# Kernel optimization log

Hardware: AMD Instinct MI355X
Metric: run time of the kernel (lower is better)

## Reference

```python
import jax, jax.numpy as jnp
import numpy as np

L, D, H, V, B, S = 12, 768, 12, 50257, 1, 2048
F = 4 * D
HD = D // H
EPS = 1e-5
NEG = -1e38


def setup_inputs() -> dict:
    key = jax.random.key(0)
    ks = jax.random.split(key, 12)
    s = 0.02
    f32 = jnp.float32
    return {
        "x": jax.random.normal(ks[0], (B, S, D), f32),
        "ln1_g": jnp.ones((L, D), f32), "ln1_b": jnp.zeros((L, D), f32),
        "Wq": jax.random.normal(ks[1], (L, D, D), f32) * s,
        "Wk": jax.random.normal(ks[2], (L, D, D), f32) * s,
        "Wv": jax.random.normal(ks[3], (L, D, D), f32) * s,
        "Wo": jax.random.normal(ks[4], (L, D, D), f32) * s,
        "bo": jnp.zeros((L, D), f32),
        "ln2_g": jnp.ones((L, D), f32), "ln2_b": jnp.zeros((L, D), f32),
        "Wfc": jax.random.normal(ks[5], (L, D, F), f32) * s,
        "bfc": jnp.zeros((L, F), f32),
        "Wp": jax.random.normal(ks[6], (L, F, D), f32) * s,
        "bp": jnp.zeros((L, D), f32),
        "lnf_g": jnp.ones((D,), f32), "lnf_b": jnp.zeros((D,), f32),
        "Wlm": jax.random.normal(ks[7], (D, V), f32) * s,
    }


def _ln(h, g, b):
    mu = h.mean(-1, keepdims=True)
    var = ((h - mu) ** 2).mean(-1, keepdims=True)
    return (h - mu) * jax.lax.rsqrt(var + EPS) * g + b


def reference(x, ln1_g, ln1_b, Wq, Wk, Wv, Wo, bo, ln2_g, ln2_b,
              Wfc, bfc, Wp, bp, lnf_g, lnf_b, Wlm):
    Bx, Sx, Dx = x.shape
    # additive causal mask, NOTE: original has no 1/sqrt(head_dim) scaling
    mask = (1.0 - jnp.tril(jnp.ones((Sx, Sx), x.dtype))) * NEG

    def block(h, p):
        g1, b1, wq, wk, wv, wo, bo_, g2, b2, wfc, bfc_, wp, bp_ = p
        hn = _ln(h, g1, b1)
        def heads(w):  # [B,S,D] -> [B,H,S,hd]
            return (hn @ w).reshape(Bx, Sx, H, HD).transpose(0, 2, 1, 3)
        q, k, v = heads(wq), heads(wk), heads(wv)
        scores = jnp.einsum('bhqd,bhkd->bhqk', q, k) + mask
        probs = jax.nn.softmax(scores, axis=-1)
        attn = jnp.einsum('bhqk,bhkd->bhqd', probs, v)
        attn = attn.transpose(0, 2, 1, 3).reshape(Bx, Sx, Dx)
        h = h + attn @ wo + bo_
        hn2 = _ln(h, g2, b2)
        ff = jax.nn.gelu(hn2 @ wfc + bfc_, approximate=False) @ wp + bp_
        return h + ff, None

    h, _ = jax.lax.scan(
        block, x,
        (ln1_g, ln1_b, Wq, Wk, Wv, Wo, bo, ln2_g, ln2_b, Wfc, bfc, Wp, bp))
    return _ln(h, lnf_g, lnf_b) @ Wlm
```

## Files before the change

kernel.cpp:

```cpp
#include <hip/hip_runtime.h>
#include <hip/hip_bf16.h>
#include <math.h>

typedef unsigned short ushort;
typedef __attribute__((ext_vector_type(8))) short short8;
typedef __attribute__((ext_vector_type(4))) short short4v;
typedef __attribute__((ext_vector_type(4))) float f4v;

constexpr int SEQ = 2048;
constexpr int DM  = 768;
constexpr int NH  = 12;
constexpr int HDM = 64;
constexpr int FF  = 3072;
constexpr int NL  = 12;
constexpr int NV  = 50257;
constexpr int NVP = 50432;

__device__ inline ushort f2bf(float f) {
    union { float f; unsigned u; } v; v.f = f;
    unsigned r = v.u + 0x7fffu + ((v.u >> 16) & 1u);
    return (ushort)(r >> 16);
}

__device__ __forceinline__ void gld16(const ushort* g, ushort* l) {
    __builtin_amdgcn_global_load_lds(
        (const __attribute__((address_space(1))) void*)g,
        (__attribute__((address_space(3))) void*)l, 16, 0, 0);
}

__global__ __launch_bounds__(256) void ln_kernel(const float* __restrict__ x,
                                                 const float* __restrict__ g,
                                                 const float* __restrict__ b,
                                                 ushort* __restrict__ out) {
    int row = blockIdx.x;
    int t = threadIdx.x;
    const float* xr = x + (size_t)row * DM;
    float v0 = xr[t], v1 = xr[t + 256], v2 = xr[t + 512];
    float s = v0 + v1 + v2;
    float s2 = v0 * v0 + v1 * v1 + v2 * v2;
    for (int m = 1; m < 64; m <<= 1) { s += __shfl_xor(s, m); s2 += __shfl_xor(s2, m); }
    __shared__ float ls[4], ls2[4];
    int w = t >> 6;
    if ((t & 63) == 0) { ls[w] = s; ls2[w] = s2; }
    __syncthreads();
    s = ls[0] + ls[1] + ls[2] + ls[3];
    s2 = ls2[0] + ls2[1] + ls2[2] + ls2[3];
    float mu = s * (1.0f / DM);
    float var = s2 * (1.0f / DM) - mu * mu;
    float rs = rsqrtf(var + 1e-5f);
    ushort* o = out + (size_t)row * DM;
    o[t]       = f2bf((v0 - mu) * rs * g[t]       + b[t]);
    o[t + 256] = f2bf((v1 - mu) * rs * g[t + 256] + b[t + 256]);
    o[t + 512] = f2bf((v2 - mu) * rs * g[t + 512] + b[t + 512]);
}

struct CvtArgs {
    const float* src[7];
    ushort*      dst[7];
    long inL[7], outL[7];
    int  K[7], N[7], tk[7], tn[7];
    int  base[8];
};

__global__ __launch_bounds__(256) void cvt_all(CvtArgs a) {
    __shared__ ushort T[64][72];
    int idx = blockIdx.x;
    int seg = 0;
    #pragma unroll
    for (int i = 1; i < 7; ++i) if (idx >= a.base[i]) seg = i;
    int local = idx - a.base[seg];
    int K = a.K[seg], N = a.N[seg];
    int tk = a.tk[seg], tn = a.tn[seg];
    int k_t = local % tk;
    int rst = local / tk;
    int n_t = rst % tn;
    int l   = rst / tn;
    const float* ip = a.src[seg] + (size_t)l * a.inL[seg];
    ushort* op      = a.dst[seg] + (size_t)l * a.outL[seg];
    int kb = k_t * 64, nb = n_t * 64;
    int t = threadIdx.x;
    int nl = t & 63, ks = (t >> 6) * 16;
    int n = nb + nl;
    #pragma unroll
    for (int j = 0; j < 16; ++j) {
        float f = (n < N) ? ip[(size_t)(kb + ks + j) * N + n] : 0.f;
        T[nl][ks + j] = f2bf(f);
    }
    __syncthreads();
    int r = t >> 2, c4 = (t & 3) * 16;
    *(short8*)(op + (size_t)(nb + r) * K + kb + c4)     = *(const short8*)&T[r][c4];
    *(short8*)(op + (size_t)(nb + r) * K + kb + c4 + 8) = *(const short8*)&T[r][c4 + 8];
}

template <int BM, int BN, int EPI, bool DB, bool SWZ>
__global__ __launch_bounds__(256, 2) void gemmT(const ushort* __restrict__ A,
                                                const ushort* __restrict__ Bt,
                                                const float* __restrict__ bias,
                                                const float* __restrict__ res,
                                                void* __restrict__ outp,
                                                ushort* __restrict__ vt,
                                                int M, int N, int K, int ldOut) {
    constexpr int FM = BM / 32;
    constexpr int FN = BN / 32;
    constexpr int NBUF = DB ? 2 : 1;
    constexpr int ASZ = BM * 64;
    constexpr int BSZ = BN * 64;
    __shared__ ushort As[NBUF * ASZ];
    __shared__ ushort Bs[NBUF * BSZ];
    int tid = threadIdx.x, lane = tid & 63, wave = tid >> 6;
    int wm = (wave >> 1) * (BM / 2), wn = (wave & 1) * (BN / 2);
    int mBase, nBase;
    if constexpr (SWZ) {
        int gx = gridDim.x;
        int nwg = gx * gridDim.y;
        int flat = blockIdx.y * gx + blockIdx.x;
        int xcd = flat & 7, idx = flat >> 3;
        int q = nwg >> 3, r = nwg & 7;
        int wg = (xcd < r ? xcd * (q + 1) : r * (q + 1) + (xcd - r) * q) + idx;
        mBase = (wg % gx) * BM;
        nBase = (wg / gx) * BN;
    } else {
        mBase = blockIdx.x * BM;
        nBase = blockIdx.y * BN;
    }
    int lr = lane & 15, lg = lane >> 4;
    int swz = (lr & 7) << 3;

    f4v acc[FM][FN];
    #pragma unroll
    for (int i = 0; i < FM; ++i)
        #pragma unroll
        for (int j = 0; j < FN; ++j) acc[i][j] = (f4v){0.f, 0.f, 0.f, 0.f};

    int cBase = wave * 64 + lane;

    auto stage = [&](int kb, int buf) {
        #pragma unroll
        for (int i = 0; i < BM / 32; ++i) {
            int c = i * 256 + cBase;
            int row = c >> 3;
            int kc = (c & 7) ^ (row & 7);
            gld16(A + (size_t)(mBase + row) * K + kb + kc * 8,
                  As + buf * ASZ + (size_t)(i * 256 + wave * 64) * 8);
        }
        #pragma unroll
        for (int i = 0; i < BN / 32; ++i) {
            int c = i * 256 + cBase;
            int row = c >> 3;
            int kc = (c & 7) ^ (row & 7);
            gld16(Bt + (size_t)(nBase + row) * K + kb + kc * 8,
                  Bs + buf * BSZ + (size_t)(i * 256 + wave * 64) * 8);
        }
    };
    auto compute = [&](int buf) {
        #pragma unroll
        for (int kk = 0; kk < 2; ++kk) {
            short8 a[FM], b[FN];
            #pragma unroll
            for (int fr = 0; fr < FM; ++fr)
                a[fr] = *(const short8*)(As + buf * ASZ + (wm + fr * 16 + lr) * 64 + ((((kk * 4 + lg) << 3)) ^ swz));
            #pragma unroll
            for (int fc = 0; fc < FN; ++fc)
                b[fc] = *(const short8*)(Bs + buf * BSZ + (wn + fc * 16 + lr) * 64 + ((((kk * 4 + lg) << 3)) ^ swz));
            #pragma unroll
            for (int fr = 0; fr < FM; ++fr)
                #pragma unroll
                for (int fc = 0; fc < FN; ++fc)
                    acc[fr][fc] = __builtin_amdgcn_mfma_f32_16x16x32_bf16(a[fr], b[fc], acc[fr][fc], 0, 0, 0);
        }
    };

    if constexpr (DB) {
        stage(0, 0);
        __syncthreads();
        int cur = 0;
        for (int kb = 0; kb < K; kb += 64) {
            if (kb + 64 < K) stage(kb + 64, cur ^ 1);
            compute(cur);
            __syncthreads();
            cur ^= 1;
        }
    } else {
        for (int kb = 0; kb < K; kb += 64) {
            stage(kb, 0);
            __syncthreads();
            compute(0);
            __syncthreads();
        }
    }

    if constexpr (EPI == 4) {
        if (nBase < 1536) {
            #pragma unroll
            for (int fr = 0; fr < FM; ++fr)
                #pragma unroll
                for (int fc = 0; fc < FN; ++fc)
                    #pragma unroll
                    for (int r = 0; r < 4; ++r) {
                        int row = mBase + wm + fr * 16 + 4 * lg + r;
                        int col = nBase + wn + fc * 16 + lr;
                        ((ushort*)outp)[(size_t)row * ldOut + col] = f2bf(acc[fr][fc][r]);
                    }
        } else {
            #pragma unroll
            for (int fr = 0; fr < FM; ++fr)
                #pragma unroll
                for (int fc = 0; fc < FN; ++fc) {
                    short4v pk;
                    #pragma unroll
                    for (int r = 0; r < 4; ++r) pk[r] = (short)f2bf(acc[fr][fc][r]);
                    int d  = nBase - 1536 + wn + fc * 16 + lr;
                    int m0 = mBase + wm + fr * 16 + 4 * lg;
                    *(short4v*)(vt + (size_t)d * SEQ + m0) = pk;
                }
        }
        return;
    }

    #pragma unroll
    for (int fr = 0; fr < FM; ++fr)
        #pragma unroll
        for (int fc = 0; fc < FN; ++fc)
            #pragma unroll
            for (int r = 0; r < 4; ++r) {
                int row = mBase + wm + fr * 16 + 4 * lg + r;
                int col = nBase + wn + fc * 16 + lr;
                float v = acc[fr][fc][r];
                if constexpr (EPI == 0) {
                    ((ushort*)outp)[(size_t)row * ldOut + col] = f2bf(v);
                } else if constexpr (EPI == 1) {
                    v += bias[col] + res[(size_t)row * ldOut + col];
                    ((float*)outp)[(size_t)row * ldOut + col] = v;
                } else if constexpr (EPI == 2) {
                    v += bias[col];
                    v = 0.5f * v * (1.f + erff(v * 0.70710678118f));
                    ((ushort*)outp)[(size_t)row * ldOut + col] = f2bf(v);
                } else {
                    if (col < N) ((float*)outp)[(size_t)row * ldOut + col] = v;
                }
            }
}

__global__ __launch_bounds__(128) void attn_v7(const ushort* __restrict__ Qg,
                                               const ushort* __restrict__ Kg,
                                               const ushort* __restrict__ Vt,
                                               ushort* __restrict__ Og) {
    __shared__ ushort Ks[2 * 4096];
    __shared__ ushort Vs[2 * 4096];
    __shared__ ushort Ps[2 * 1024];
    int tid = threadIdx.x, lane = tid & 63, wave = tid >> 6;
    int flat = blockIdx.x;
    int qt   = (SEQ / 32) - 1 - (flat / NH);
    int head = flat % NH;
    int lr = lane & 15, lg = lane >> 4;
    int qr0 = qt * 32 + wave * 16;
    int hoff = head * HDM;
    int swz = (lr & 7) << 3;
    int ktiles = (qt * 32 + 31) / 64 + 1;

    short8 qf0 = *(const short8*)(Qg + (size_t)(qr0 + lr) * 2304 + hoff + lg * 8);
    short8 qf1 = *(const short8*)(Qg + (size_t)(qr0 + lr) * 2304 + hoff + 32 + lg * 8);

    const f4v fz = {0.f, 0.f, 0.f, 0.f};
    f4v o[4];
    o[0] = fz; o[1] = fz; o[2] = fz; o[3] = fz;
    float mrow[4] = {-1e30f, -1e30f, -1e30f, -1e30f};
    float lsum[4] = {0.f, 0.f, 0.f, 0.f};

    auto stageKV = [&](int kb, int buf) {
        #pragma unroll
        for (int j = 0; j < 4; ++j) {
            int cc = j * 128 + wave * 64 + lane;
            int row = cc >> 3;
            int kc = (cc & 7) ^ (row & 7);
            gld16(Kg + (size_t)(kb * 64 + row) * 2304 + hoff + kc * 8,
                  Ks + buf * 4096 + (size_t)(j * 128 + wave * 64) * 8);
            gld16(Vt + (size_t)(hoff + row) * SEQ + kb * 64 + kc * 8,
                  Vs + buf * 4096 + (size_t)(j * 128 + wave * 64) * 8);
        }
    };

    stageKV(0, 0);
    __syncthreads();
    int cur = 0;

    for (int kb = 0; kb < ktiles; ++kb) {
        if (kb + 1 < ktiles) stageKV(kb + 1, cur ^ 1);

        f4v s[4];
        #pragma unroll
        for (int n = 0; n < 4; ++n) {
            const ushort* kr = Ks + cur * 4096 + (n * 16 + lr) * 64;
            short8 k0 = *(const short8*)(kr + ((lg << 3) ^ swz));
            short8 k1 = *(const short8*)(kr + ((((4 + lg) << 3)) ^ swz));
            f4v z = fz;
            z = __builtin_amdgcn_mfma_f32_16x16x32_bf16(qf0, k0, z, 0, 0, 0);
            s[n] = __builtin_amdgcn_mfma_f32_16x16x32_bf16(qf1, k1, z, 0, 0, 0);
        }
        if (kb == ktiles - 1) {
            #pragma unroll
            for (int n = 0; n < 4; ++n)
                #pragma unroll
                for (int r = 0; r < 4; ++r) {
                    int col = kb * 64 + n * 16 + lr;
                    int row = qr0 + 4 * lg + r;
                    if (col > row) s[n][r] = -1e38f;
                }
        }

        int sub = lr & 7, hi = lr >> 3;
        #pragma unroll
        for (int r = 0; r < 4; ++r) {
            float mx = fmaxf(fmaxf(s[0][r], s[1][r]), fmaxf(s[2][r], s[3][r]));
            mx = fmaxf(mx, __shfl_xor(mx, 1));
            mx = fmaxf(mx, __shfl_xor(mx, 2));
            mx = fmaxf(mx, __shfl_xor(mx, 4));
            mx = fmaxf(mx, __shfl_xor(mx, 8));
            float mnew = fmaxf(mrow[r], mx);
            float corr = __expf(mrow[r] - mnew);
            float ps0 = __expf(s[0][r] - mnew);
            float ps1 = __expf(s[1][r] - mnew);
            float ps2 = __expf(s[2][r] - mnew);
            float ps3 = __expf(s[3][r] - mnew);
            float rs = ps0 + ps1 + ps2 + ps3;
            rs += __shfl_xor(rs, 1);
            rs += __shfl_xor(rs, 2);
            rs += __shfl_xor(rs, 4);
            rs += __shfl_xor(rs, 8);
            lsum[r] = lsum[r] * corr + rs;
            mrow[r] = mnew;
            o[0][r] *= corr; o[1][r] *= corr; o[2][r] *= corr; o[3][r] *= corr;
            int prow = 4 * lg + r;
            ushort* pb = Ps + wave * 1024 + prow * 64;
            int px = prow & 7;
            pb[(((0 + hi) ^ px) << 3) | sub] = f2bf(ps0);
            pb[(((2 + hi) ^ px) << 3) | sub] = f2bf(ps1);
            pb[(((4 + hi) ^ px) << 3) | sub] = f2bf(ps2);
            pb[(((6 + hi) ^ px) << 3) | sub] = f2bf(ps3);
        }
        __syncthreads();

        #pragma unroll
        for (int kk = 0; kk < 2; ++kk) {
            short8 pa = *(const short8*)(Ps + wave * 1024 + lr * 64 + ((((kk * 4 + lg) << 3)) ^ swz));
            #pragma unroll
            for (int dn = 0; dn < 4; ++dn) {
                short8 vb = *(const short8*)(Vs + cur * 4096 + (dn * 16 + lr) * 64 + ((((kk * 4 + lg) << 3)) ^ swz));
                o[dn] = __builtin_amdgcn_mfma_f32_16x16x32_bf16(pa, vb, o[dn], 0, 0, 0);
            }
        }
        __syncthreads();
        cur ^= 1;
    }

    #pragma unroll
    for (int dn = 0; dn < 4; ++dn)
        #pragma unroll
        for (int r = 0; r < 4; ++r) {
            int row = qr0 + 4 * lg + r;
            Og[(size_t)row * DM + hoff + dn * 16 + lr] = f2bf(o[dn][r] / lsum[r]);
        }
}

template <int EPI>
__global__ __launch_bounds__(256) void gemm64(const ushort* __restrict__ A,
                                              const float* __restrict__ B,
                                              const float* __restrict__ bias,
                                              const float* __restrict__ res,
                                              void* __restrict__ outp,
                                              int M, int N, int K) {
    __shared__ ushort As[64][64];
    __shared__ ushort Bs[64][72];
    int tid = threadIdx.x;
    int lane = tid & 63, wave = tid >> 6;
    int wm = (wave >> 1) * 32, wn = (wave & 1) * 32;
    int mBase = blockIdx.x * 64, nBase = blockIdx.y * 64;
    int lr = lane & 15, lg = lane >> 4;

    const f4v fz = {0.f, 0.f, 0.f, 0.f};
    f4v acc[2][2];
    acc[0][0] = fz; acc[0][1] = fz; acc[1][0] = fz; acc[1][1] = fz;

    int ar = tid >> 2, ac = (tid & 3) * 16;
    int br = tid >> 2, bc = (tid & 3) * 16;

    for (int kb = 0; kb < K; kb += 64) {
        const short8* ag = (const short8*)(A + (size_t)(mBase + ar) * K + kb + ac);
        *(short8*)&As[ar][ac]     = ag[0];
        *(short8*)&As[ar][ac + 8] = ag[1];
        if constexpr (EPI == 3) {
            #pragma unroll
            for (int j = 0; j < 16; ++j) {
                int col = nBase + bc + j;
                float f = (col < N) ? B[(size_t)(kb + br) * N + col] : 0.f;
                Bs[bc + j][br] = f2bf(f);
            }
        } else {
            const float4* bg = (const float4*)(B + (size_t)(kb + br) * N + nBase + bc);
            float fv[16];
            *(float4*)&fv[0]  = bg[0];
            *(float4*)&fv[4]  = bg[1];
            *(float4*)&fv[8]  = bg[2];
            *(float4*)&fv[12] = bg[3];
            #pragma unroll
            for (int j = 0; j < 16; ++j) Bs[bc + j][br] = f2bf(fv[j]);
        }
        __syncthreads();
        #pragma unroll
        for (int kk = 0; kk < 2; ++kk) {
            short8 a0 = *(const short8*)&As[wm + lr][kk * 32 + lg * 8];
            short8 a1 = *(const short8*)&As[wm + 16 + lr][kk * 32 + lg * 8];
            short8 b0 = *(const short8*)&Bs[wn + lr][kk * 32 + lg * 8];
            short8 b1 = *(const short8*)&Bs[wn + 16 + lr][kk * 32 + lg * 8];
            acc[0][0] = __builtin_amdgcn_mfma_f32_16x16x32_bf16(a0, b0, acc[0][0], 0, 0, 0);
            acc[0][1] = __builtin_amdgcn_mfma_f32_16x16x32_bf16(a0, b1, acc[0][1], 0, 0, 0);
            acc[1][0] = __builtin_amdgcn_mfma_f32_16x16x32_bf16(a1, b0, acc[1][0], 0, 0, 0);
            acc[1][1] = __builtin_amdgcn_mfma_f32_16x16x32_bf16(a1, b1, acc[1][1], 0, 0, 0);
        }
        __syncthreads();
    }

    #pragma unroll
    for (int fm = 0; fm < 2; ++fm)
        #pragma unroll
        for (int fn = 0; fn < 2; ++fn)
            #pragma unroll
            for (int r = 0; r < 4; ++r) {
                int row = mBase + wm + fm * 16 + 4 * lg + r;
                int col = nBase + wn + fn * 16 + lr;
                float v = acc[fm][fn][r];
                if constexpr (EPI == 0) {
                    ((ushort*)outp)[(size_t)row * N + col] = f2bf(v);
                } else if constexpr (EPI == 1) {
                    v += bias[col] + res[(size_t)row * N + col];
                    ((float*)outp)[(size_t)row * N + col] = v;
                } else if constexpr (EPI == 2) {
                    v += bias[col];
                    v = 0.5f * v * (1.f + erff(v * 0.70710678118f));
                    ((ushort*)outp)[(size_t)row * N + col] = f2bf(v);
                } else {
                    if (col < N) ((float*)outp)[(size_t)row * N + col] = v;
                }
            }
}

__global__ __launch_bounds__(256) void attn_stage(const ushort* __restrict__ Qg,
                                                  const ushort* __restrict__ Kg,
                                                  const ushort* __restrict__ Vg,
                                                  ushort* __restrict__ Og,
                                                  int ld) {
    __shared__ ushort Ks[64][64];
    __shared__ ushort Vs[64][72];
    __shared__ ushort Ps[4][16][64];
    int tid = threadIdx.x, lane = tid & 63, wave = tid >> 6;
    int qb = blockIdx.x, head = blockIdx.y;
    int lr = lane & 15, lg = lane >> 4;
    int qr0 = qb * 64 + wave * 16;
    size_t hoff = (size_t)head * HDM;

    short8 qf0 = *(const short8*)(Qg + (size_t)(qr0 + lr) * ld + hoff + lg * 8);
    short8 qf1 = *(const short8*)(Qg + (size_t)(qr0 + lr) * ld + hoff + 32 + lg * 8);

    const f4v fz = {0.f, 0.f, 0.f, 0.f};
    f4v o[4];
    o[0] = fz; o[1] = fz; o[2] = fz; o[3] = fz;
    float mrow[4] = {-1e30f, -1e30f, -1e30f, -1e30f};
    float lsum[4] = {0.f, 0.f, 0.f, 0.f};

    int r_ = tid >> 2, c_ = (tid & 3) * 16;

    for (int kb = 0; kb <= qb; ++kb) {
        const short8* kg = (const short8*)(Kg + (size_t)(kb * 64 + r_) * ld + hoff + c_);
        *(short8*)&Ks[r_][c_]     = kg[0];
        *(short8*)&Ks[r_][c_ + 8] = kg[1];
        const short8* vg = (const short8*)(Vg + (size_t)(kb * 64 + r_) * ld + hoff + c_);
        short8 v0 = vg[0], v1 = vg[1];
        #pragma unroll
        for (int j = 0; j < 8; ++j) {
            Vs[c_ + j][r_]     = (ushort)v0[j];
            Vs[c_ + 8 + j][r_] = (ushort)v1[j];
        }
        __syncthreads();

        f4v s[4];
        #pragma unroll
        for (int n = 0; n < 4; ++n) {
            short8 k0 = *(const short8*)&Ks[n * 16 + lr][lg * 8];
            short8 k1 = *(const short8*)&Ks[n * 16 + lr][32 + lg * 8];
            f4v z = fz;
            z = __builtin_amdgcn_mfma_f32_16x16x32_bf16(qf0, k0, z, 0, 0, 0);
            s[n] = __builtin_amdgcn_mfma_f32_16x16x32_bf16(qf1, k1, z, 0, 0, 0);
        }
        if (kb == qb) {
            #pragma unroll
            for (int n = 0; n < 4; ++n)
                #pragma unroll
                for (int r = 0; r < 4; ++r) {
                    int col = kb * 64 + n * 16 + lr;
                    int row = qr0 + 4 * lg + r;
                    if (col > row) s[n][r] = -1e38f;
                }
        }

        #pragma unroll
        for (int r = 0; r < 4; ++r) {
            float mx = fmaxf(fmaxf(s[0][r], s[1][r]), fmaxf(s[2][r], s[3][r]));
            mx = fmaxf(mx, __shfl_xor(mx, 1));
            mx = fmaxf(mx, __shfl_xor(mx, 2));
            mx = fmaxf(mx, __shfl_xor(mx, 4));
            mx = fmaxf(mx, __shfl_xor(mx, 8));
            float mnew = fmaxf(mrow[r], mx);
            float corr = __expf(mrow[r] - mnew);
            float ps0 = __expf(s[0][r] - mnew);
            float ps1 = __expf(s[1][r] - mnew);
            float ps2 = __expf(s[2][r] - mnew);
            float ps3 = __expf(s[3][r] - mnew);
            float rs = ps0 + ps1 + ps2 + ps3;
            rs += __shfl_xor(rs, 1);
            rs += __shfl_xor(rs, 2);
            rs += __shfl_xor(rs, 4);
            rs += __shfl_xor(rs, 8);
            lsum[r] = lsum[r] * corr + rs;
            mrow[r] = mnew;
            o[0][r] *= corr; o[1][r] *= corr; o[2][r] *= corr; o[3][r] *= corr;
            Ps[wave][4 * lg + r][0 * 16 + lr] = f2bf(ps0);
            Ps[wave][4 * lg + r][1 * 16 + lr] = f2bf(ps1);
            Ps[wave][4 * lg + r][2 * 16 + lr] = f2bf(ps2);
            Ps[wave][4 * lg + r][3 * 16 + lr] = f2bf(ps3);
        }
        __syncthreads();

        #pragma unroll
        for (int kk = 0; kk < 2; ++kk) {
            short8 pa = *(const short8*)&Ps[wave][lr][kk * 32 + lg * 8];
            #pragma unroll
            for (int dn = 0; dn < 4; ++dn) {
                short8 vb = *(const short8*)&Vs[dn * 16 + lr][kk * 32 + lg * 8];
                o[dn] = __builtin_amdgcn_mfma_f32_16x16x32_bf16(pa, vb, o[dn], 0, 0, 0);
            }
        }
        __syncthreads();
    }

    #pragma unroll
    for (int dn = 0; dn < 4; ++dn)
        #pragma unroll
        for (int r = 0; r < 4; ++r) {
            int row = qr0 + 4 * lg + r;
            Og[(size_t)row * DM + hoff + dn * 16 + lr] = f2bf(o[dn][r] / lsum[r]);
        }
}

extern "C" void kernel_launch(void* const* d_in, const int* in_sizes, int n_in,
                              void* d_out, int out_size, void* d_ws, size_t ws_size,
                              hipStream_t stream) {
    const float* x     = (const float*)d_in[0];
    const float* ln1_g = (const float*)d_in[1];
    const float* ln1_b = (const float*)d_in[2];
    const float* Wq    = (const float*)d_in[3];
    const float* Wk    = (const float*)d_in[4];
    const float* Wv    = (const float*)d_in[5];
    const float* Wo    = (const float*)d_in[6];
    const float* bo    = (const float*)d_in[7];
    const float* ln2_g = (const float*)d_in[8];
    const float* ln2_b = (const float*)d_in[9];
    const float* Wfc   = (const float*)d_in[10];
    const float* bfc   = (const float*)d_in[11];
    const float* Wp    = (const float*)d_in[12];
    const float* bp    = (const float*)d_in[13];
    const float* lnf_g = (const float*)d_in[14];
    const float* lnf_b = (const float*)d_in[15];
    const float* Wlm   = (const float*)d_in[16];

    dim3 blk(256);

    size_t offs[12];
    size_t need = 0;
    size_t sizes[11] = {
        (size_t)SEQ * DM * 4,
        (size_t)SEQ * DM * 2,
        (size_t)SEQ * 2304 * 2,
        (size_t)SEQ * DM * 2,
        (size_t)SEQ * FF * 2,
        (size_t)DM * SEQ * 2,
        (size_t)NL * 2304 * DM * 2,
        (size_t)NL * DM * DM * 2,
        (size_t)NL * FF * DM * 2,
        (size_t)NL * DM * FF * 2,
        (size_t)NVP * DM * 2,
    };
    for (int i = 0; i < 11; ++i) { offs[i] = need; need += sizes[i]; }
    offs[11] = need;

    if (ws_size >= need) {
        char* ws = (char*)d_ws;
        float*  h    = (float*)(ws + offs[0]);
        ushort* hn   = (ushort*)(ws + offs[1]);
        ushort* qkv  = (ushort*)(ws + offs[2]);
        ushort* ab_  = (ushort*)(ws + offs[3]);
        ushort* fb_  = (ushort*)(ws + offs[4]);
        ushort* vt   = (ushort*)(ws + offs[5]);
        ushort* qkvw = (ushort*)(ws + offs[6]);
        ushort* wow  = (ushort*)(ws + offs[7]);
        ushort* fcw  = (ushort*)(ws + offs[8]);
        ushort* wpw  = (ushort*)(ws + offs[9]);
        ushort* lmw  = (ushort*)(ws + offs[10]);

        hipMemcpyAsync(h, x, (size_t)SEQ * DM * 4, hipMemcpyDeviceToDevice, stream);

        CvtArgs ca;
        const float* srcs[7] = {Wq, Wk, Wv, Wo, Wfc, Wp, Wlm};
        ushort* dsts[7] = {qkvw, qkvw + DM * DM, qkvw + 2 * DM * DM, wow, fcw, wpw, lmw};
        long inLs[7]  = {(long)DM * DM, (long)DM * DM, (long)DM * DM, (long)DM * DM,
                         (long)DM * FF, (long)FF * DM, 0};
        long outLs[7] = {(long)2304 * DM, (long)2304 * DM, (long)2304 * DM, (long)DM * DM,
                         (long)FF * DM, (long)DM * FF, 0};
        int Ks_[7] = {DM, DM, DM, DM, DM, FF, DM};
        int Ns_[7] = {DM, DM, DM, DM, FF, DM, NV};
        int tks[7] = {12, 12, 12, 12, 12, 48, 12};
        int tns[7] = {12, 12, 12, 12, 48, 12, NVP / 64};
        int lays[7] = {NL, NL, NL, NL, NL, NL, 1};
        int total = 0;
        for (int i = 0; i < 7; ++i) {
            ca.src[i] = srcs[i]; ca.dst[i] = dsts[i];
            ca.inL[i] = inLs[i]; ca.outL[i] = outLs[i];
            ca.K[i] = Ks_[i]; ca.N[i] = Ns_[i]; ca.tk[i] = tks[i]; ca.tn[i] = tns[i];
            ca.base[i] = total;
            total += tks[i] * tns[i] * lays[i];
        }
        ca.base[7] = total;
        cvt_all<<<dim3(total), blk, 0, stream>>>(ca);

        for (int l = 0; l < NL; ++l) {
            const ushort* qw = qkvw + (size_t)l * 2304 * DM;
            ln_kernel<<<SEQ, blk, 0, stream>>>(h, ln1_g + l * DM, ln1_b + l * DM, hn);
            gemmT<64, 64, 4, true, false><<<dim3(32, 36), blk, 0, stream>>>(hn, qw, nullptr, nullptr, qkv, vt, SEQ, 2304, DM, 2304);
            attn_v7<<<dim3((SEQ / 32) * NH), dim3(128), 0, stream>>>(qkv, qkv + 768, vt, ab_);
            gemmT<64, 64, 1, true, false><<<dim3(32, 12), blk, 0, stream>>>(ab_, wow + (size_t)l * DM * DM, bo + l * DM, h, h, nullptr, SEQ, DM, DM, DM);
            ln_kernel<<<SEQ, blk, 0, stream>>>(h, ln2_g + l * DM, ln2_b + l * DM, hn);
            gemmT<64, 64, 2, true, false><<<dim3(32, 48), blk, 0, stream>>>(hn, fcw + (size_t)l * FF * DM, bfc + l * FF, nullptr, fb_, nullptr, SEQ, FF, DM, FF);
            gemmT<64, 64, 1, true, false><<<dim3(32, 12), blk, 0, stream>>>(fb_, wpw + (size_t)l * DM * FF, bp + l * DM, h, h, nullptr, SEQ, DM, FF, DM);
        }
        ln_kernel<<<SEQ, blk, 0, stream>>>(h, lnf_g, lnf_b, hn);
        gemmT<128, 256, 3, false, true><<<dim3(16, NVP / 256), blk, 0, stream>>>(hn, lmw, nullptr, nullptr, d_out, nullptr, SEQ, NV, DM, NV);
        return;
    }

    char* ws = (char*)d_ws;
    float*  h   = (float*)ws;   ws += (size_t)SEQ * DM * 4;
    ushort* hn  = (ushort*)ws;  ws += (size_t)SEQ * DM * 2;
    ushort* qb_ = (ushort*)ws;  ws += (size_t)SEQ * DM * 2;
    ushort* kb_ = (ushort*)ws;  ws += (size_t)SEQ * DM * 2;
    ushort* vb_ = (ushort*)ws;  ws += (size_t)SEQ * DM * 2;
    ushort* ab_ = (ushort*)ws;  ws += (size_t)SEQ * DM * 2;
    ushort* fb_ = (ushort*)ws;  ws += (size_t)SEQ * FF * 2;

    hipMemcpyAsync(h, x, (size_t)SEQ * DM * 4, hipMemcpyDeviceToDevice, stream);

    dim3 gdd(SEQ / 64, DM / 64);
    dim3 gdf(SEQ / 64, FF / 64);
    dim3 gda(SEQ / 64, NH);
    dim3 gdl(SEQ / 64, (NV + 63) / 64);

    for (int l = 0; l < NL; ++l) {
        ln_kernel<<<SEQ, blk, 0, stream>>>(h, ln1_g + l * DM, ln1_b + l * DM, hn);
        gemm64<0><<<gdd, blk, 0, stream>>>(hn, Wq + (size_t)l * DM * DM, nullptr, nullptr, qb_, SEQ, DM, DM);
        gemm64<0><<<gdd, blk, 0, stream>>>(hn, Wk + (size_t)l * DM * DM, nullptr, nullptr, kb_, SEQ, DM, DM);
        gemm64<0><<<gdd, blk, 0, stream>>>(hn, Wv + (size_t)l * DM * DM, nullptr, nullptr, vb_, SEQ, DM, DM);
        attn_stage<<<gda, blk, 0, stream>>>(qb_, kb_, vb_, ab_, DM);
        gemm64<1><<<gdd, blk, 0, stream>>>(ab_, Wo + (size_t)l * DM * DM, bo + l * DM, h, h, SEQ, DM, DM);
        ln_kernel<<<SEQ, blk, 0, stream>>>(h, ln2_g + l * DM, ln2_b + l * DM, hn);
        gemm64<2><<<gdf, blk, 0, stream>>>(hn, Wfc + (size_t)l * DM * FF, bfc + l * FF, nullptr, fb_, SEQ, FF, DM);
        gemm64<1><<<gdd, blk, 0, stream>>>(fb_, Wp + (size_t)l * FF * DM, bp + l * DM, h, h, SEQ, DM, FF);
    }
    ln_kernel<<<SEQ, blk, 0, stream>>>(h, lnf_g, lnf_b, hn);
    gemm64<3><<<gdl, blk, 0, stream>>>(hn, Wlm, nullptr, nullptr, d_out, SEQ, NV, DM);
}
```

Baseline: 2.518 ms.

## Split-K the FFN down-projection and retile the LM-head GEMM

```diff
diff --git a/kernel.cpp b/kernel.cpp
--- a/kernel.cpp
+++ b/kernel.cpp
@@ -14,7 +14,7 @@
 constexpr int FF  = 3072;
 constexpr int NL  = 12;
 constexpr int NV  = 50257;
-constexpr int NVP = 50432;
+constexpr int NVP = 50496;
 
 __device__ inline ushort f2bf(float f) {
     union { float f; unsigned u; } v; v.f = f;
@@ -54,6 +54,24 @@
     o[t + 512] = f2bf((v2 - mu) * rs * g[t + 512] + b[t + 512]);
 }
 
+__global__ __launch_bounds__(256) void spk_reduce(const float* __restrict__ p,
+                                                  const float* __restrict__ bias,
+                                                  float* __restrict__ h) {
+    int idx = blockIdx.x * 256 + threadIdx.x;
+    int col4 = idx % (DM / 4);
+    float4 a  = ((const float4*)h)[idx];
+    float4 b  = ((const float4*)bias)[col4];
+    float4 s0 = ((const float4*)p)[idx];
+    float4 s1 = ((const float4*)(p + (size_t)SEQ * DM))[idx];
+    float4 s2 = ((const float4*)(p + 2 * (size_t)SEQ * DM))[idx];
+    float4 s3 = ((const float4*)(p + 3 * (size_t)SEQ * DM))[idx];
+    a.x += b.x + s0.x + s1.x + s2.x + s3.x;
+    a.y += b.y + s0.y + s1.y + s2.y + s3.y;
+    a.z += b.z + s0.z + s1.z + s2.z + s3.z;
+    a.w += b.w + s0.w + s1.w + s2.w + s3.w;
+    ((float4*)h)[idx] = a;
+}
+
 struct CvtArgs {
     const float* src[7];
     ushort*      dst[7];
@@ -92,14 +110,15 @@
     *(short8*)(op + (size_t)(nb + r) * K + kb + c4 + 8) = *(const short8*)&T[r][c4 + 8];
 }
 
-template <int BM, int BN, int EPI, bool DB, bool SWZ>
-__global__ __launch_bounds__(256, 2) void gemmT(const ushort* __restrict__ A,
-                                                const ushort* __restrict__ Bt,
-                                                const float* __restrict__ bias,
-                                                const float* __restrict__ res,
-                                                void* __restrict__ outp,
-                                                ushort* __restrict__ vt,
-                                                int M, int N, int K, int ldOut) {
+template <int BM, int BN, int EPI, bool DB, bool SWZ, int MINW>
+__global__ __launch_bounds__(256, MINW) void gemmT(const ushort* __restrict__ A,
+                                                   const ushort* __restrict__ Bt,
+                                                   const float* __restrict__ bias,
+                                                   const float* __restrict__ res,
+                                                   void* __restrict__ outp,
+                                                   ushort* __restrict__ vt,
+                                                   int M, int N, int K,
+                                                   int kLen, int ldOut) {
     constexpr int FM = BM / 32;
     constexpr int FN = BN / 32;
     constexpr int NBUF = DB ? 2 : 1;
@@ -123,6 +142,7 @@
         mBase = blockIdx.x * BM;
         nBase = blockIdx.y * BN;
     }
+    int kOff = kLen * blockIdx.z;
     int lr = lane & 15, lg = lane >> 4;
     int swz = (lr & 7) << 3;
 
@@ -140,7 +160,7 @@
             int c = i * 256 + cBase;
             int row = c >> 3;
             int kc = (c & 7) ^ (row & 7);
-            gld16(A + (size_t)(mBase + row) * K + kb + kc * 8,
+            gld16(A + (size_t)(mBase + row) * K + kOff + kb + kc * 8,
                   As + buf * ASZ + (size_t)(i * 256 + wave * 64) * 8);
         }
         #pragma unroll
@@ -148,7 +168,7 @@
             int c = i * 256 + cBase;
             int row = c >> 3;
             int kc = (c & 7) ^ (row & 7);
-            gld16(Bt + (size_t)(nBase + row) * K + kb + kc * 8,
+            gld16(Bt + (size_t)(nBase + row) * K + kOff + kb + kc * 8,
                   Bs + buf * BSZ + (size_t)(i * 256 + wave * 64) * 8);
         }
     };
@@ -174,14 +194,14 @@
         stage(0, 0);
         __syncthreads();
         int cur = 0;
-        for (int kb = 0; kb < K; kb += 64) {
-            if (kb + 64 < K) stage(kb + 64, cur ^ 1);
+        for (int kb = 0; kb < kLen; kb += 64) {
+            if (kb + 64 < kLen) stage(kb + 64, cur ^ 1);
             compute(cur);
             __syncthreads();
             cur ^= 1;
         }
     } else {
-        for (int kb = 0; kb < K; kb += 64) {
+        for (int kb = 0; kb < kLen; kb += 64) {
             stage(kb, 0);
             __syncthreads();
             compute(0);
@@ -216,6 +236,9 @@
         }
         return;
     }
+
+    float* out3 = (float*)outp;
+    if constexpr (EPI == 3) out3 += (size_t)blockIdx.z * M * ldOut;
 
     #pragma unroll
     for (int fr = 0; fr < FM; ++fr)
@@ -236,7 +259,7 @@
                     v = 0.5f * v * (1.f + erff(v * 0.70710678118f));
                     ((ushort*)outp)[(size_t)row * ldOut + col] = f2bf(v);
                 } else {
-                    if (col < N) ((float*)outp)[(size_t)row * ldOut + col] = v;
+                    if (col < N) out3[(size_t)row * ldOut + col] = v;
                 }
             }
 }
@@ -574,9 +597,9 @@
 
     dim3 blk(256);
 
-    size_t offs[12];
+    size_t offs[13];
     size_t need = 0;
-    size_t sizes[11] = {
+    size_t sizes[12] = {
         (size_t)SEQ * DM * 4,
         (size_t)SEQ * DM * 2,
         (size_t)SEQ * 2304 * 2,
@@ -588,11 +611,14 @@
         (size_t)NL * FF * DM * 2,
         (size_t)NL * DM * FF * 2,
         (size_t)NVP * DM * 2,
+        (size_t)4 * SEQ * DM * 4,
     };
-    for (int i = 0; i < 11; ++i) { offs[i] = need; need += sizes[i]; }
-    offs[11] = need;
-
-    if (ws_size >= need) {
+    for (int i = 0; i < 12; ++i) { offs[i] = need; need += sizes[i]; }
+    offs[12] = need;
+    size_t need_base = offs[11];
+    bool useSpk = (ws_size >= need);
+
+    if (ws_size >= need_base) {
         char* ws = (char*)d_ws;
         float*  h    = (float*)(ws + offs[0]);
         ushort* hn   = (ushort*)(ws + offs[1]);
@@ -605,6 +631,7 @@
         ushort* fcw  = (ushort*)(ws + offs[8]);
         ushort* wpw  = (ushort*)(ws + offs[9]);
         ushort* lmw  = (ushort*)(ws + offs[10]);
+        float*  spk  = (float*)(ws + offs[11]);
 
         hipMemcpyAsync(h, x, (size_t)SEQ * DM * 4, hipMemcpyDeviceToDevice, stream);
 
@@ -634,15 +661,20 @@
         for (int l = 0; l < NL; ++l) {
             const ushort* qw = qkvw + (size_t)l * 2304 * DM;
             ln_kernel<<<SEQ, blk, 0, stream>>>(h, ln1_g + l * DM, ln1_b + l * DM, hn);
-            gemmT<64, 64, 4, true, false><<<dim3(32, 36), blk, 0, stream>>>(hn, qw, nullptr, nullptr, qkv, vt, SEQ, 2304, DM, 2304);
+            gemmT<64, 64, 4, true, false, 2><<<dim3(32, 36), blk, 0, stream>>>(hn, qw, nullptr, nullptr, qkv, vt, SEQ, 2304, DM, DM, 2304);
             attn_v7<<<dim3((SEQ / 32) * NH), dim3(128), 0, stream>>>(qkv, qkv + 768, vt, ab_);
-            gemmT<64, 64, 1, true, false><<<dim3(32, 12), blk, 0, stream>>>(ab_, wow + (size_t)l * DM * DM, bo + l * DM, h, h, nullptr, SEQ, DM, DM, DM);
+            gemmT<64, 64, 1, true, false, 2><<<dim3(32, 12), blk, 0, stream>>>(ab_, wow + (size_t)l * DM * DM, bo + l * DM, h, h, nullptr, SEQ, DM, DM, DM, DM);
             ln_kernel<<<SEQ, blk, 0, stream>>>(h, ln2_g + l * DM, ln2_b + l * DM, hn);
-            gemmT<64, 64, 2, true, false><<<dim3(32, 48), blk, 0, stream>>>(hn, fcw + (size_t)l * FF * DM, bfc + l * FF, nullptr, fb_, nullptr, SEQ, FF, DM, FF);
-            gemmT<64, 64, 1, true, false><<<dim3(32, 12), blk, 0, stream>>>(fb_, wpw + (size_t)l * DM * FF, bp + l * DM, h, h, nullptr, SEQ, DM, FF, DM);
+            gemmT<64, 64, 2, true, false, 2><<<dim3(32, 48), blk, 0, stream>>>(hn, fcw + (size_t)l * FF * DM, bfc + l * FF, nullptr, fb_, nullptr, SEQ, FF, DM, DM, FF);
+            if (useSpk) {
+                gemmT<64, 64, 3, true, false, 2><<<dim3(32, 12, 4), blk, 0, stream>>>(fb_, wpw + (size_t)l * DM * FF, nullptr, nullptr, spk, nullptr, SEQ, DM, FF, FF / 4, DM);
+                spk_reduce<<<dim3(SEQ * DM / 4 / 256), blk, 0, stream>>>(spk, bp + l * DM, h);
+            } else {
+                gemmT<64, 64, 1, true, false, 2><<<dim3(32, 12), blk, 0, stream>>>(fb_, wpw + (size_t)l * DM * FF, bp + l * DM, h, h, nullptr, SEQ, DM, FF, FF, DM);
+            }
         }
         ln_kernel<<<SEQ, blk, 0, stream>>>(h, lnf_g, lnf_b, hn);
-        gemmT<128, 256, 3, false, true><<<dim3(16, NVP / 256), blk, 0, stream>>>(hn, lmw, nullptr, nullptr, d_out, nullptr, SEQ, NV, DM, NV);
+        gemmT<128, 192, 3, false, true, 3><<<dim3(16, NVP / 192), blk, 0, stream>>>(hn, lmw, nullptr, nullptr, d_out, nullptr, SEQ, NV, DM, DM, NV);
         return;
     }
 
```

New measurement: 2.413 ms. 4.2% less time.
